# Kernel optimization log

Measured on AMD Instinct MI355X. Metric: run time of the kernel, lower is better.

## Reference

```python
import jax, jax.numpy as jnp
import numpy as np

B, C, L = 256, 256, 512
EPS = 1e-5

def setup_inputs() -> dict:
    key = jax.random.key(0)
    k1, k2, k3, k4 = jax.random.split(key, 4)
    x = jax.random.normal(k1, (B, C, L), dtype=jnp.float32)
    idx = jax.random.randint(k2, (B, L), 0, L + 1, dtype=jnp.int32)  # L == pad slot
    # Conv1d(2C, C, 1): weight [C, 2C], bias [C]
    W = jax.random.normal(k3, (C, 2 * C), dtype=jnp.float32) * (1.0 / np.sqrt(2 * C))
    b = jax.random.normal(k4, (C,), dtype=jnp.float32) * 0.01
    return {"x": x, "idx": idx, "W": W, "b": b}

def reference(x, idx, W, b):
    # collect_neighbours: pad length dim with one zero column, gather per (b, l)
    x_pad = jnp.pad(x, ((0, 0), (0, 0), (0, 1)))            # [B, C, L+1]
    nbr = jnp.take_along_axis(x_pad, idx[:, None, :].astype(jnp.int32), axis=2)  # [B, C, L]
    cat = jnp.concatenate([x, nbr], axis=1)                 # [B, 2C, L]
    # 1x1 Conv1d == channel matmul
    y = jnp.einsum('oc,bcl->bol', W, cat) + b[None, :, None]  # [B, C, L]
    # InstanceNorm1d (affine=False): normalize over L per (b, c), biased var
    mu = jnp.mean(y, axis=2, keepdims=True)
    var = jnp.mean(jnp.square(y - mu), axis=2, keepdims=True)
    y = (y - mu) * jax.lax.rsqrt(var + EPS)
    return jax.nn.relu(y)
```

## Files before the change

### kernel.cpp

```cpp
#include <hip/hip_runtime.h>
#include <hip/hip_bf16.h>
#include <stdint.h>

typedef __bf16 bf16x8 __attribute__((ext_vector_type(8)));
typedef float  f32x4  __attribute__((ext_vector_type(4)));

__device__ __forceinline__ uint32_t cvt2(float a, float b) {
    __hip_bfloat162 h = __float22bfloat162_rn(make_float2(a, b));
    uint32_t u; __builtin_memcpy(&u, &h, 4); return u;
}
__device__ __forceinline__ float bflo(uint32_t u) { uint32_t t = u << 16;         float f; __builtin_memcpy(&f, &t, 4); return f; }
__device__ __forceinline__ float bfhi(uint32_t u) { uint32_t t = u & 0xffff0000u; float f; __builtin_memcpy(&f, &t, 4); return f; }
__device__ __forceinline__ int swz(int u) { return u ^ ((u >> 3) & 7); }

__global__ __launch_bounds__(256, 4)
void pack_transpose(const float* __restrict__ x, const float* __restrict__ W,
                    unsigned short* __restrict__ xT, unsigned short* __restrict__ wT)
{
    const int tid = threadIdx.x;
    const int id  = blockIdx.x;
    if (id < 2048) {
        const int b = id >> 3, kc = id & 7;
        const int s2 = tid >> 6, l4 = tid & 63;
        const float* src0 = x + ((size_t)b << 17) + ((size_t)((kc << 5) + (s2 << 3)) << 9);
        unsigned short* dst0 = xT + (((size_t)(b << 5) + (kc << 2) + s2) << 12);
        #pragma unroll
        for (int lh = 0; lh < 2; ++lh) {
            const int l0 = (lh << 8) + (l4 << 2);
            float4 xr[8];
            #pragma unroll
            for (int j = 0; j < 8; ++j)
                xr[j] = *(const float4*)(src0 + (j << 9) + l0);
            #pragma unroll
            for (int lv = 0; lv < 4; ++lv) {
                uint4 p;
                p.x = cvt2((&xr[0].x)[lv], (&xr[1].x)[lv]);
                p.y = cvt2((&xr[2].x)[lv], (&xr[3].x)[lv]);
                p.z = cvt2((&xr[4].x)[lv], (&xr[5].x)[lv]);
                p.w = cvt2((&xr[6].x)[lv], (&xr[7].x)[lv]);
                *(uint4*)(dst0 + ((l0 + lv) << 3)) = p;
            }
        }
    } else {
        const int og = id - 2048;
        const int r = tid & 63, sg = tid >> 6;
        const float* wrow = W + ((size_t)((og << 5) + (r & 31)) << 9) + ((r >> 5) << 8);
        #pragma unroll
        for (int ss = 0; ss < 8; ++ss) {
            const int s = (sg << 3) + ss;
            float4 f0 = *(const float4*)(wrow + (s << 3));
            float4 f1 = *(const float4*)(wrow + (s << 3) + 4);
            uint4 p;
            p.x = cvt2(f0.x, f0.y); p.y = cvt2(f0.z, f0.w);
            p.z = cvt2(f1.x, f1.y); p.w = cvt2(f1.z, f1.w);
            *(uint4*)(wT + (((((og << 5) + s) << 6) + r) << 3)) = p;
        }
    }
}

__global__ __launch_bounds__(256, 2)
void edge_gemm(const unsigned short* __restrict__ xT,
               const unsigned short* __restrict__ wT,
               const int* __restrict__ idx,
               float* __restrict__ out)
{
    __shared__ __align__(16) unsigned char smem[37888];
    unsigned short* y2 = (unsigned short*)smem;
    float* red         = (float*)(smem + 36864);

    const int tid  = threadIdx.x;
    const int wv   = tid >> 6;
    const int lane = tid & 63;
    const int m    = lane & 15;
    const int q    = lane >> 4;

    const int id  = blockIdx.x;
    const int rem = id & 63;
    const int b   = ((id >> 6) << 3) + (rem & 7);
    const int og  = rem >> 3;
    const int o0  = og << 5;

    const unsigned short* xb = xT + ((size_t)b << 17);
    const unsigned short* wb = wT + (og << 14);

    int iv[8];
    #pragma unroll
    for (int nt = 0; nt < 8; ++nt)
        iv[nt] = idx[((size_t)b << 9) + (wv << 7) + (nt << 4) + m];

    f32x4 acc[4][8];
    #pragma unroll
    for (int mt = 0; mt < 4; ++mt)
        #pragma unroll
        for (int nt = 0; nt < 8; ++nt)
            acc[mt][nt] = (f32x4){0.f, 0.f, 0.f, 0.f};

    #pragma unroll
    for (int kc = 0; kc < 8; ++kc) {
        const int s = (kc << 2) + q;
        bf16x8 av[4], bv[8];
        const unsigned short* ab = wb + (s << 9) + (m << 3);
        #pragma unroll
        for (int mt = 0; mt < 4; ++mt)
            av[mt] = *(const bf16x8*)(ab + (mt << 7));
        const unsigned short* bb = xb + (s << 12) + (((wv << 7) + m) << 3);
        #pragma unroll
        for (int nt = 0; nt < 8; ++nt)
            bv[nt] = *(const bf16x8*)(bb + (nt << 7));
        #pragma unroll
        for (int mt = 0; mt < 4; ++mt)
            #pragma unroll
            for (int nt = 0; nt < 8; ++nt)
                acc[mt][nt] = __builtin_amdgcn_mfma_f32_16x16x32_bf16(av[mt], bv[nt], acc[mt][nt], 0, 0, 0);
    }

    #pragma unroll
    for (int mt = 2; mt < 4; ++mt)
        #pragma unroll
        for (int nt = 0; nt < 8; ++nt) {
            int col  = (wv << 7) + (nt << 4) + m;
            int row0 = ((mt - 2) << 4) + (q << 2);
            uint2 p;
            p.x = cvt2(acc[mt][nt][0], acc[mt][nt][1]);
            p.y = cvt2(acc[mt][nt][2], acc[mt][nt][3]);
            *(uint2*)(y2 + col * 36 + row0) = p;
        }
    __syncthreads();

    float vvl[2][8][4];
    float s_[2][4], q_[2][4];
    #pragma unroll
    for (int mt = 0; mt < 2; ++mt)
        #pragma unroll
        for (int r4 = 0; r4 < 4; ++r4) { s_[mt][r4] = 0.f; q_[mt][r4] = 0.f; }

    #pragma unroll
    for (int nt = 0; nt < 8; ++nt) {
        int  c   = iv[nt];
        bool inb = (c < 512);
        int  cc  = inb ? c : 0;
        #pragma unroll
        for (int mt = 0; mt < 2; ++mt) {
            uint2 g = *(const uint2*)(y2 + cc * 36 + (mt << 4) + (q << 2));
            float gv[4];
            gv[0] = inb ? bflo(g.x) : 0.f;
            gv[1] = inb ? bfhi(g.x) : 0.f;
            gv[2] = inb ? bflo(g.y) : 0.f;
            gv[3] = inb ? bfhi(g.y) : 0.f;
            #pragma unroll
            for (int r4 = 0; r4 < 4; ++r4) {
                float val = acc[mt][nt][r4] + gv[r4];
                vvl[mt][nt][r4] = val;
                s_[mt][r4] += val;
                q_[mt][r4] += val * val;
            }
        }
    }

    #pragma unroll
    for (int mt = 0; mt < 2; ++mt)
        #pragma unroll
        for (int r4 = 0; r4 < 4; ++r4) {
            float s = s_[mt][r4], ss = q_[mt][r4];
            #pragma unroll
            for (int off = 1; off < 16; off <<= 1) {
                s  += __shfl_xor(s,  off, 64);
                ss += __shfl_xor(ss, off, 64);
            }
            if (m == 0) {
                int r = (mt << 4) + (q << 2) + r4;
                red[(r << 3) + (wv << 1)]     = s;
                red[(r << 3) + (wv << 1) + 1] = ss;
            }
        }
    __syncthreads();

    #pragma unroll
    for (int mt = 0; mt < 2; ++mt)
        #pragma unroll
        for (int r4 = 0; r4 < 4; ++r4) {
            int r = (mt << 4) + (q << 2) + r4;
            float S = red[(r << 3)]     + red[(r << 3) + 2] + red[(r << 3) + 4] + red[(r << 3) + 6];
            float Q = red[(r << 3) + 1] + red[(r << 3) + 3] + red[(r << 3) + 5] + red[(r << 3) + 7];
            float mu  = S * (1.0f / 512.0f);
            float var = Q * (1.0f / 512.0f) - mu * mu;
            float rs  = rsqrtf(var + 1e-5f);
            float* op = out + (((size_t)(b << 8) + o0 + r) << 9) + (wv << 7) + m;
            #pragma unroll
            for (int nt = 0; nt < 8; ++nt) {
                float t = (vvl[mt][nt][r4] - mu) * rs;
                op[nt << 4] = fmaxf(t, 0.0f);
            }
        }
}

__global__ __launch_bounds__(256, 2)
void edgeconv_fused(const float* __restrict__ x,
                    const int*   __restrict__ idx,
                    const float* __restrict__ W,
                    float*       __restrict__ out)
{
    __shared__ __align__(16) unsigned char smem[65536];
    unsigned short* wlds = (unsigned short*)smem;
    unsigned short* xT   = (unsigned short*)(smem + 32768);
    unsigned short* y2   = (unsigned short*)smem;
    float*          red  = (float*)(smem + 38912);

    const int tid  = threadIdx.x;
    const int wv   = tid >> 6;
    const int lane = tid & 63;
    const int m    = lane & 15;
    const int q    = lane >> 4;

    const int id  = blockIdx.x;
    const int rem = id & 63;
    const int b   = ((id >> 6) << 3) + (rem & 7);
    const int o0  = (rem >> 3) << 5;

    const float* xb = x + ((size_t)b << 17);

    #pragma unroll
    for (int i = 0; i < 16; ++i) {
        int r = (i << 2) + wv;
        const float4 f = *(const float4*)(W + ((size_t)(o0 + (r & 31)) << 9)
                                            + ((r >> 5) << 8) + (lane << 2));
        uint2 p; p.x = cvt2(f.x, f.y); p.y = cvt2(f.z, f.w);
        int sl = lane >> 1;
        *(uint2*)(wlds + (sl << 9) + ((swz(r) ^ (sl & 7)) << 3) + ((lane & 1) << 2)) = p;
    }

    f32x4 acc[4][8];
    #pragma unroll
    for (int mt = 0; mt < 4; ++mt)
        #pragma unroll
        for (int nt = 0; nt < 8; ++nt)
            acc[mt][nt] = (f32x4){0.f, 0.f, 0.f, 0.f};

    float4 xr0[8], xr1[8];
    auto loadg = [&](int kc, int g, float4* xr) {
        int gid = (g << 8) + tid;
        int s2  = gid >> 7;
        int l4  = gid & 127;
        const float* base = xb + ((size_t)((kc << 5) + (s2 << 3)) << 9) + (l4 << 2);
        #pragma unroll
        for (int j = 0; j < 8; ++j) xr[j] = *(const float4*)(base + (j << 9));
    };
    auto storeg = [&](int g, const float4* xr) {
        int gid = (g << 8) + tid;
        int s2  = gid >> 7;
        int l4  = gid & 127;
        #pragma unroll
        for (int lv = 0; lv < 4; ++lv) {
            int l = (l4 << 2) + lv;
            uint4 p;
            p.x = cvt2((&xr[0].x)[lv], (&xr[1].x)[lv]);
            p.y = cvt2((&xr[2].x)[lv], (&xr[3].x)[lv]);
            p.z = cvt2((&xr[4].x)[lv], (&xr[5].x)[lv]);
            p.w = cvt2((&xr[6].x)[lv], (&xr[7].x)[lv]);
            *(uint4*)(xT + (s2 << 12) + (swz(l) << 3)) = p;
        }
    };

    loadg(0, 0, xr0);
    loadg(0, 1, xr1);
    storeg(0, xr0);
    storeg(1, xr1);
    __syncthreads();

    for (int kc = 0; kc < 8; ++kc) {
        if (kc < 7) loadg(kc + 1, 0, xr0);

        bf16x8 av[4], bv[8];
        #pragma unroll
        for (int mt = 0; mt < 4; ++mt) {
            int sl = (kc << 2) + q;
            av[mt] = *(const bf16x8*)(wlds + (sl << 9) + ((swz((mt << 4) + m) ^ (sl & 7)) << 3));
        }
        #pragma unroll
        for (int nt = 0; nt < 8; ++nt)
            bv[nt] = *(const bf16x8*)(xT + (q << 12) + (swz((wv << 7) + (nt << 4) + m) << 3));

        #pragma unroll
        for (int mt = 0; mt < 4; ++mt)
            #pragma unroll
            for (int nt = 0; nt < 8; ++nt)
                acc[mt][nt] = __builtin_amdgcn_mfma_f32_16x16x32_bf16(av[mt], bv[nt], acc[mt][nt], 0, 0, 0);

        if (kc < 7) loadg(kc + 1, 1, xr1);
        __syncthreads();
        if (kc < 7) {
            storeg(0, xr0);
            storeg(1, xr1);
            __syncthreads();
        }
    }

    int iv[8];
    #pragma unroll
    for (int nt = 0; nt < 8; ++nt)
        iv[nt] = idx[((size_t)b << 9) + (wv << 7) + (nt << 4) + m];

    #pragma unroll
    for (int mt = 2; mt < 4; ++mt)
        #pragma unroll
        for (int nt = 0; nt < 8; ++nt) {
            int col  = (wv << 7) + (nt << 4) + m;
            int row0 = ((mt - 2) << 4) + (q << 2);
            uint2 p;
            p.x = cvt2(acc[mt][nt][0], acc[mt][nt][1]);
            p.y = cvt2(acc[mt][nt][2], acc[mt][nt][3]);
            *(uint2*)(y2 + col * 36 + row0) = p;
        }
    __syncthreads();

    float vvl[2][8][4];
    float s_[2][4], q_[2][4];
    #pragma unroll
    for (int mt = 0; mt < 2; ++mt)
        #pragma unroll
        for (int r4 = 0; r4 < 4; ++r4) { s_[mt][r4] = 0.f; q_[mt][r4] = 0.f; }

    #pragma unroll
    for (int nt = 0; nt < 8; ++nt) {
        int  c   = iv[nt];
        bool inb = (c < 512);
        int  cc  = inb ? c : 0;
        #pragma unroll
        for (int mt = 0; mt < 2; ++mt) {
            uint2 g = *(const uint2*)(y2 + cc * 36 + (mt << 4) + (q << 2));
            float gv[4];
            gv[0] = inb ? bflo(g.x) : 0.f;
            gv[1] = inb ? bfhi(g.x) : 0.f;
            gv[2] = inb ? bflo(g.y) : 0.f;
            gv[3] = inb ? bfhi(g.y) : 0.f;
            #pragma unroll
            for (int r4 = 0; r4 < 4; ++r4) {
                float val = acc[mt][nt][r4] + gv[r4];
                vvl[mt][nt][r4] = val;
                s_[mt][r4] += val;
                q_[mt][r4] += val * val;
            }
        }
    }

    #pragma unroll
    for (int mt = 0; mt < 2; ++mt)
        #pragma unroll
        for (int r4 = 0; r4 < 4; ++r4) {
            float s = s_[mt][r4], ss = q_[mt][r4];
            #pragma unroll
            for (int off = 1; off < 16; off <<= 1) {
                s  += __shfl_xor(s,  off, 64);
                ss += __shfl_xor(ss, off, 64);
            }
            if (m == 0) {
                int r = (mt << 4) + (q << 2) + r4;
                red[(r << 3) + (wv << 1)]     = s;
                red[(r << 3) + (wv << 1) + 1] = ss;
            }
        }
    __syncthreads();

    #pragma unroll
    for (int mt = 0; mt < 2; ++mt)
        #pragma unroll
        for (int r4 = 0; r4 < 4; ++r4) {
            int r = (mt << 4) + (q << 2) + r4;
            float S = red[(r << 3)]     + red[(r << 3) + 2] + red[(r << 3) + 4] + red[(r << 3) + 6];
            float Q = red[(r << 3) + 1] + red[(r << 3) + 3] + red[(r << 3) + 5] + red[(r << 3) + 7];
            float mu  = S * (1.0f / 512.0f);
            float var = Q * (1.0f / 512.0f) - mu * mu;
            float rs  = rsqrtf(var + 1e-5f);
            float* op = out + (((size_t)(b << 8) + o0 + r) << 9) + (wv << 7) + m;
            #pragma unroll
            for (int nt = 0; nt < 8; ++nt) {
                float t = (vvl[mt][nt][r4] - mu) * rs;
                op[nt << 4] = fmaxf(t, 0.0f);
            }
        }
}

extern "C" void kernel_launch(void* const* d_in, const int* in_sizes, int n_in,
                              void* d_out, int out_size, void* d_ws, size_t ws_size,
                              hipStream_t stream) {
    const float* x   = (const float*)d_in[0];
    const int*   idx = (const int*)  d_in[1];
    const float* W   = (const float*)d_in[2];
    float* out = (float*)d_out;

    const size_t xT_bytes = (size_t)256 * 32 * 512 * 8 * 2;
    const size_t wT_bytes = (size_t)8 * 32 * 64 * 8 * 2;

    if (ws_size >= xT_bytes + wT_bytes) {
        unsigned short* xT = (unsigned short*)d_ws;
        unsigned short* wT = (unsigned short*)((char*)d_ws + xT_bytes);
        pack_transpose<<<dim3(2056), dim3(256), 0, stream>>>(x, W, xT, wT);
        edge_gemm<<<dim3(2048), dim3(256), 0, stream>>>(xT, wT, idx, out);
    } else {
        edgeconv_fused<<<dim3(2048), dim3(256), 0, stream>>>(x, idx, W, out);
    }
}
```

Measured before the change: 301.9 us.

## Stage GEMM operands through double-buffered LDS with direct global-to-LDS loads

The edge_gemm kernel now copies each K-chunk of packed x and W from global memory straight into LDS with global_load_lds, double-buffered so the next chunk loads while MFMAs run on the current one. This replaces direct per-lane global vector loads of operands. The pack kernel remaps block ids so batches are grouped, and it uses nontemporal loads; output stores are also nontemporal. LDS use rises to 72KB per block, which may limit occupancy. The LDS reads are unswizzled and may cause bank conflicts.

```diff
diff --git a/kernel.cpp b/kernel.cpp
--- a/kernel.cpp
+++ b/kernel.cpp
@@ -12,6 +12,13 @@
 __device__ __forceinline__ float bflo(uint32_t u) { uint32_t t = u << 16;         float f; __builtin_memcpy(&f, &t, 4); return f; }
 __device__ __forceinline__ float bfhi(uint32_t u) { uint32_t t = u & 0xffff0000u; float f; __builtin_memcpy(&f, &t, 4); return f; }
 __device__ __forceinline__ int swz(int u) { return u ^ ((u >> 3) & 7); }
+
+__device__ __forceinline__ void gload_lds16(const void* g, void* l) {
+    __builtin_amdgcn_global_load_lds(
+        (const __attribute__((address_space(1))) uint32_t*)g,
+        (__attribute__((address_space(3))) uint32_t*)l,
+        16, 0, 0);
+}
 
 __global__ __launch_bounds__(256, 4)
 void pack_transpose(const float* __restrict__ x, const float* __restrict__ W,
@@ -20,24 +27,25 @@
     const int tid = threadIdx.x;
     const int id  = blockIdx.x;
     if (id < 2048) {
-        const int b = id >> 3, kc = id & 7;
+        const int b  = ((id >> 6) << 3) + (id & 7);
+        const int kc = (id >> 3) & 7;
         const int s2 = tid >> 6, l4 = tid & 63;
         const float* src0 = x + ((size_t)b << 17) + ((size_t)((kc << 5) + (s2 << 3)) << 9);
         unsigned short* dst0 = xT + (((size_t)(b << 5) + (kc << 2) + s2) << 12);
         #pragma unroll
         for (int lh = 0; lh < 2; ++lh) {
             const int l0 = (lh << 8) + (l4 << 2);
-            float4 xr[8];
+            f32x4 xr[8];
             #pragma unroll
             for (int j = 0; j < 8; ++j)
-                xr[j] = *(const float4*)(src0 + (j << 9) + l0);
+                xr[j] = __builtin_nontemporal_load((const f32x4*)(src0 + (j << 9) + l0));
             #pragma unroll
             for (int lv = 0; lv < 4; ++lv) {
                 uint4 p;
-                p.x = cvt2((&xr[0].x)[lv], (&xr[1].x)[lv]);
-                p.y = cvt2((&xr[2].x)[lv], (&xr[3].x)[lv]);
-                p.z = cvt2((&xr[4].x)[lv], (&xr[5].x)[lv]);
-                p.w = cvt2((&xr[6].x)[lv], (&xr[7].x)[lv]);
+                p.x = cvt2(xr[0][lv], xr[1][lv]);
+                p.y = cvt2(xr[2][lv], xr[3][lv]);
+                p.z = cvt2(xr[4][lv], xr[5][lv]);
+                p.w = cvt2(xr[6][lv], xr[7][lv]);
                 *(uint4*)(dst0 + ((l0 + lv) << 3)) = p;
             }
         }
@@ -64,7 +72,7 @@
                const int* __restrict__ idx,
                float* __restrict__ out)
 {
-    __shared__ __align__(16) unsigned char smem[37888];
+    __shared__ __align__(16) unsigned char smem[73728];
     unsigned short* y2 = (unsigned short*)smem;
     float* red         = (float*)(smem + 36864);
 
@@ -80,8 +88,10 @@
     const int og  = rem >> 3;
     const int o0  = og << 5;
 
-    const unsigned short* xb = xT + ((size_t)b << 17);
-    const unsigned short* wb = wT + (og << 14);
+    const char* xb = (const char*)xT + ((size_t)b << 18);
+    const char* wb = (const char*)wT + (og << 15);
+
+    const int offS = (wv << 10) + (lane << 4);
 
     int iv[8];
     #pragma unroll
@@ -95,23 +105,43 @@
         for (int nt = 0; nt < 8; ++nt)
             acc[mt][nt] = (f32x4){0.f, 0.f, 0.f, 0.f};
 
+    {
+        char* Bl = (char*)smem;
+        #pragma unroll
+        for (int i = 0; i < 8; ++i)
+            gload_lds16(xb + (i << 12) + offS, Bl + (i << 12) + offS);
+        gload_lds16(wb + offS, Bl + 32768 + offS);
+    }
+    __syncthreads();
+
     #pragma unroll
     for (int kc = 0; kc < 8; ++kc) {
-        const int s = (kc << 2) + q;
+        const int cur = kc & 1;
+        if (kc < 7) {
+            char* Bl = (char*)smem + (cur ^ 1) * 36864;
+            const char* Bg = xb + ((kc + 1) << 15);
+            #pragma unroll
+            for (int i = 0; i < 8; ++i)
+                gload_lds16(Bg + (i << 12) + offS, Bl + (i << 12) + offS);
+            gload_lds16(wb + ((kc + 1) << 12) + offS, Bl + 32768 + offS);
+        }
+
+        const unsigned short* B0 = (const unsigned short*)(smem + cur * 36864);
+        const unsigned short* A0 = B0 + 16384;
         bf16x8 av[4], bv[8];
-        const unsigned short* ab = wb + (s << 9) + (m << 3);
         #pragma unroll
         for (int mt = 0; mt < 4; ++mt)
-            av[mt] = *(const bf16x8*)(ab + (mt << 7));
-        const unsigned short* bb = xb + (s << 12) + (((wv << 7) + m) << 3);
+            av[mt] = *(const bf16x8*)(A0 + (q << 9) + (((mt << 4) + m) << 3));
         #pragma unroll
         for (int nt = 0; nt < 8; ++nt)
-            bv[nt] = *(const bf16x8*)(bb + (nt << 7));
+            bv[nt] = *(const bf16x8*)(B0 + (q << 12) + (((wv << 7) + (nt << 4) + m) << 3));
         #pragma unroll
         for (int mt = 0; mt < 4; ++mt)
             #pragma unroll
             for (int nt = 0; nt < 8; ++nt)
                 acc[mt][nt] = __builtin_amdgcn_mfma_f32_16x16x32_bf16(av[mt], bv[nt], acc[mt][nt], 0, 0, 0);
+
+        if (kc < 7) __syncthreads();
     }
 
     #pragma unroll
@@ -189,7 +219,7 @@
             #pragma unroll
             for (int nt = 0; nt < 8; ++nt) {
                 float t = (vvl[mt][nt][r4] - mu) * rs;
-                op[nt << 4] = fmaxf(t, 0.0f);
+                __builtin_nontemporal_store(fmaxf(t, 0.0f), op + (nt << 4));
             }
         }
 }
@@ -202,7 +232,7 @@
 {
     __shared__ __align__(16) unsigned char smem[65536];
     unsigned short* wlds = (unsigned short*)smem;
-    unsigned short* xT   = (unsigned short*)(smem + 32768);
+    unsigned short* xTl  = (unsigned short*)(smem + 32768);
     unsigned short* y2   = (unsigned short*)smem;
     float*          red  = (float*)(smem + 38912);
 
@@ -257,7 +287,7 @@
             p.y = cvt2((&xr[2].x)[lv], (&xr[3].x)[lv]);
             p.z = cvt2((&xr[4].x)[lv], (&xr[5].x)[lv]);
             p.w = cvt2((&xr[6].x)[lv], (&xr[7].x)[lv]);
-            *(uint4*)(xT + (s2 << 12) + (swz(l) << 3)) = p;
+            *(uint4*)(xTl + (s2 << 12) + (swz(l) << 3)) = p;
         }
     };
 
@@ -278,7 +308,7 @@
         }
         #pragma unroll
         for (int nt = 0; nt < 8; ++nt)
-            bv[nt] = *(const bf16x8*)(xT + (q << 12) + (swz((wv << 7) + (nt << 4) + m) << 3));
+            bv[nt] = *(const bf16x8*)(xTl + (q << 12) + (swz((wv << 7) + (nt << 4) + m) << 3));
 
         #pragma unroll
         for (int mt = 0; mt < 4; ++mt)
```

New measurement: 287.8 us. -4.7%, faster.
